# Kernel tuning notes

Measured on AMD Instinct MI355X. Metric: run time of the kernel, lower is better.

## Reference

```python
import jax, jax.numpy as jnp
import numpy as np

DIM = 1024
NUM_HEADS = 16
DH = DIM // NUM_HEADS  # 64
B, S = 4, 2048


def setup_inputs() -> dict:
    key = jax.random.key(0)
    ks = jax.random.split(key, 9)
    sc = 0.02
    x = jax.random.normal(ks[0], (B, S, DIM), dtype=jnp.float32)
    # per-head projection weights stacked: [H, DIM, DH] (input-major layout)
    Wq = jax.random.normal(ks[1], (NUM_HEADS, DIM, DH), dtype=jnp.float32) * sc
    Wk = jax.random.normal(ks[2], (NUM_HEADS, DIM, DH), dtype=jnp.float32) * sc
    Wv = jax.random.normal(ks[3], (NUM_HEADS, DIM, DH), dtype=jnp.float32) * sc
    bq = jax.random.normal(ks[4], (NUM_HEADS, DH), dtype=jnp.float32) * sc
    bk = jax.random.normal(ks[5], (NUM_HEADS, DH), dtype=jnp.float32) * sc
    bv = jax.random.normal(ks[6], (NUM_HEADS, DH), dtype=jnp.float32) * sc
    Wo = jax.random.normal(ks[7], (DIM, DIM), dtype=jnp.float32) * sc  # (in, out)
    bo = jax.random.normal(ks[8], (DIM,), dtype=jnp.float32) * sc
    return {"x": x, "Wq": Wq, "Wk": Wk, "Wv": Wv,
            "bq": bq, "bk": bk, "bv": bv, "Wo": Wo, "bo": bo}


def reference(x, Wq, Wk, Wv, bq, bk, bv, Wo, bo):
    # Per-head Linear projections, vectorized over heads: [B,H,S,DH]
    q = jnp.einsum('bsd,hde->bhse', x, Wq) + bq[None, :, None, :]
    k = jnp.einsum('bsd,hde->bhse', x, Wk) + bk[None, :, None, :]
    v = jnp.einsum('bsd,hde->bhse', x, Wv) + bv[None, :, None, :]
    # attention_matmul: Q @ K^T normalized by sqrt(dim_per_head)
    scale = 1.0 / jnp.sqrt(jnp.asarray(DH, dtype=x.dtype))
    scores = jnp.einsum('bhse,bhte->bhst', q, k) * scale  # [B,H,S,S]
    attn = jax.nn.softmax(scores, axis=-1)
    # attn_drop with p=0.0 is identity
    o = jnp.einsum('bhst,bhte->bhse', attn, v)  # [B,H,S,DH]
    # concat along last dim in head order -> [B,S,H*DH]
    o = jnp.transpose(o, (0, 2, 1, 3)).reshape(x.shape[0], x.shape[1], NUM_HEADS * DH)
    # output projection (proj_drop p=0.0 is identity)
    return o @ Wo + bo
```

## Files before the change

kernel.cpp:

```cpp
#include <hip/hip_runtime.h>
#include <stdint.h>

#define DIM 1024
#define NH 16
#define DH 64
#define BATCH 4
#define SEQ 2048
#define MROWS (BATCH*SEQ)

typedef _Float16 half8 __attribute__((ext_vector_type(8)));
typedef __fp16 fp16x2 __attribute__((ext_vector_type(2)));
typedef float f32x4 __attribute__((ext_vector_type(4)));
typedef float f32x16 __attribute__((ext_vector_type(16)));
typedef unsigned int u32x2 __attribute__((ext_vector_type(2)));

__device__ __forceinline__ unsigned short f2h(float f) {
    union { _Float16 h; unsigned short u; } c; c.h = (_Float16)f; return c.u;
}
__device__ __forceinline__ unsigned int pk2u(float a, float b) {
    union { fp16x2 h; unsigned int u; } c;
    c.h = __builtin_amdgcn_cvt_pkrtz(a, b);
    return c.u;
}
__device__ __forceinline__ float fexp2(float x) {
    return __builtin_amdgcn_exp2f(x);
}
__device__ __forceinline__ void gl_lds16(const unsigned short* g, unsigned short* l) {
    __builtin_amdgcn_global_load_lds(
        (__attribute__((address_space(1))) void*)(void*)g,
        (__attribute__((address_space(3))) void*)(void*)l,
        16, 0, 0);
}


__global__ void cast_x_kernel(const float* __restrict__ x,
                              unsigned short* __restrict__ xh, int n4) {
    int i = blockIdx.x * blockDim.x + threadIdx.x;
    if (i >= n4) return;
    float4 v = reinterpret_cast<const float4*>(x)[i];
    uint2 o;
    o.x = pk2u(v.x, v.y);
    o.y = pk2u(v.z, v.w);
    reinterpret_cast<uint2*>(xh)[i] = o;
}

__global__ __launch_bounds__(256) void prep_wqkv_kernel(
    const float* __restrict__ Wq, const float* __restrict__ Wk,
    const float* __restrict__ Wv, unsigned short* __restrict__ wt)
{
    __shared__ unsigned short tile[64][65];
    const int d0 = blockIdx.x * 64;
    const int h = blockIdx.y;
    const int mat = blockIdx.z;
    const float* W = (mat == 0) ? Wq : ((mat == 1) ? Wk : Wv);
    const int c = threadIdx.x & 63;
    const int rr = threadIdx.x >> 6;
#pragma unroll
    for (int p = 0; p < 16; p++) {
        int dl = p * 4 + rr;
        tile[dl][c] = f2h(W[((size_t)h * 1024 + d0 + dl) * 64 + c]);
    }
    __syncthreads();
#pragma unroll
    for (int p = 0; p < 16; p++) {
        int el = p * 4 + rr;
        wt[(((size_t)(mat * NH + h) * 64) + el) * DIM + d0 + c] = tile[c][el];
    }
}

__global__ __launch_bounds__(256) void prep_wo_kernel(
    const float* __restrict__ Wo, unsigned short* __restrict__ wot)
{
    __shared__ unsigned short tile[64][65];
    const int d0 = blockIdx.x * 64;
    const int o0 = blockIdx.y * 64;
    const int c = threadIdx.x & 63;
    const int rr = threadIdx.x >> 6;
#pragma unroll
    for (int p = 0; p < 16; p++) {
        int dl = p * 4 + rr;
        tile[dl][c] = f2h(Wo[(size_t)(d0 + dl) * DIM + o0 + c]);
    }
    __syncthreads();
#pragma unroll
    for (int p = 0; p < 16; p++) {
        int ol = p * 4 + rr;
        wot[(size_t)(o0 + ol) * DIM + d0 + c] = tile[c][ol];
    }
}

__global__ __launch_bounds__(256) void transpose_v_kernel(
    const unsigned short* __restrict__ Vb, unsigned short* __restrict__ Vt)
{
    __shared__ unsigned short tile[64][65];
    const int s0 = blockIdx.x * 64;
    const size_t bh = (size_t)blockIdx.z * NH + blockIdx.y;
    const int c = threadIdx.x & 63;
    const int rr = threadIdx.x >> 6;
    const unsigned short* src = Vb + bh * SEQ * DH;
    unsigned short* dst = Vt + bh * DH * SEQ;
#pragma unroll
    for (int p = 0; p < 16; p++) {
        int sl = p * 4 + rr;
        tile[sl][c] = src[(size_t)(s0 + sl) * DH + c];
    }
    __syncthreads();
#pragma unroll
    for (int p = 0; p < 16; p++) {
        int dr = p * 4 + rr;
        dst[(size_t)dr * SEQ + s0 + c] = tile[c][dr];
    }
}

__global__ __launch_bounds__(256) void qkv_gemm_kernel(
    const unsigned short* __restrict__ xh,
    const unsigned short* __restrict__ wt,
    const float* __restrict__ bq, const float* __restrict__ bk,
    const float* __restrict__ bv,
    unsigned short* __restrict__ Qb,
    unsigned short* __restrict__ Kb,
    unsigned short* __restrict__ Vb)
{
    const int rowblk = blockIdx.x;
    const int hpair = blockIdx.y;
    const int mat = blockIdx.z;
    const int wave = threadIdx.x >> 6;
    const int lane = threadIdx.x & 63;
    const int quad = lane >> 4;
    const int lr = lane & 15;
    const int mhalf = wave & 1;
    const int nhalf = wave >> 1;

    __shared__ __align__(16) unsigned short Ab[2][128 * 32];
    __shared__ __align__(16) unsigned short Bt[2][128 * 32];

    const unsigned short* Asrc = xh + (size_t)rowblk * 128 * DIM;
    const unsigned short* Bsrc = wt + (size_t)(mat * NH + hpair * 2) * DH * DIM;

    const int srow = lane >> 2;
    const int scs = lane & 3;

    f32x4 acc[4][4];
#pragma unroll
    for (int mt = 0; mt < 4; mt++)
#pragma unroll
        for (int nt = 0; nt < 4; nt++) acc[mt][nt] = (f32x4){0.f, 0.f, 0.f, 0.f};

    auto stage = [&](int k0, int sel) {
#pragma unroll
        for (int jj = 0; jj < 2; jj++) {
            const int j = wave * 2 + jj;
            const int r = j * 16 + srow;
            const int cg = scs ^ ((r >> 1) & 3);
            gl_lds16(Asrc + (size_t)r * DIM + k0 + cg * 8, &Ab[sel][j * 512]);
            gl_lds16(Bsrc + (size_t)r * DIM + k0 + cg * 8, &Bt[sel][j * 512]);
        }
    };

    stage(0, 0);
    __syncthreads();

    for (int i = 0; i < DIM / 32; i++) {
        const int sel = i & 1;
        if (i + 1 < DIM / 32) stage((i + 1) * 32, sel ^ 1);

        half8 af[4], bf[4];
#pragma unroll
        for (int mt = 0; mt < 4; mt++) {
            const int row = mhalf * 64 + mt * 16 + lr;
            const int slot = quad ^ ((row >> 1) & 3);
            af[mt] = *reinterpret_cast<const half8*>(&Ab[sel][row * 32 + slot * 8]);
        }
#pragma unroll
        for (int nt = 0; nt < 4; nt++) {
            const int row = nhalf * 64 + nt * 16 + lr;
            const int slot = quad ^ ((row >> 1) & 3);
            bf[nt] = *reinterpret_cast<const half8*>(&Bt[sel][row * 32 + slot * 8]);
        }
#pragma unroll
        for (int mt = 0; mt < 4; mt++)
#pragma unroll
            for (int nt = 0; nt < 4; nt++)
                acc[mt][nt] = __builtin_amdgcn_mfma_f32_16x16x32_f16(
                    af[mt], bf[nt], acc[mt][nt], 0, 0, 0);
        __syncthreads();
    }

    const float* bias = (mat == 0) ? bq : ((mat == 1) ? bk : bv);
    const float scale = (mat == 0) ? 0.1803368801111601f : 1.0f;
    unsigned short* outp = (mat == 0) ? Qb : ((mat == 1) ? Kb : Vb);
    const int rowBase = rowblk * 128 + mhalf * 64;
    const int bb = rowBase / SEQ;
    const int sBase = rowBase % SEQ;

#pragma unroll
    for (int mt = 0; mt < 4; mt++) {
        const int s0 = sBase + mt * 16 + quad * 4;
#pragma unroll
        for (int nt = 0; nt < 4; nt++) {
            const int e = nhalf * 64 + nt * 16 + lr;
            const int head = hpair * 2 + (e >> 6);
            const int n = e & 63;
            const float bvl = bias[head * DH + n];
            const size_t base = (size_t)(bb * NH + head) * SEQ * DH;
#pragma unroll
            for (int r = 0; r < 4; r++) {
                outp[base + (size_t)(s0 + r) * DH + n] = f2h((acc[mt][nt][r] + bvl) * scale);
            }
        }
    }
}

__global__ __launch_bounds__(256, 4) void attn_kernel(
    const unsigned short* __restrict__ Qb,
    const unsigned short* __restrict__ Kb,
    const unsigned short* __restrict__ Vt,
    unsigned short* __restrict__ Ob)
{
    const int h = blockIdx.y;
    const int bb = blockIdx.z;
    const int wave = threadIdx.x >> 6;
    const int lane = threadIdx.x & 63;
    const int ql = lane & 31;
    const int hi = lane >> 5;
    const int qBase = blockIdx.x * 128 + wave * 32;

    const size_t bh = (size_t)(bb * NH + h);
    const unsigned short* Qh = Qb + bh * SEQ * DH;
    const unsigned short* Kh = Kb + bh * SEQ * DH;
    const unsigned short* Vh = Vt + bh * DH * SEQ;

    __shared__ __align__(16) unsigned short Kbuf[2][64 * 64];
    __shared__ __align__(16) unsigned short Vbuf[2][64 * 64];

    const int srow = lane >> 3;
    const int scs = lane & 7;
    const int cg = scs ^ srow;
    int koff[2], voff[2];
#pragma unroll
    for (int jj = 0; jj < 2; jj++) {
        const int r = wave * 16 + jj * 8 + srow;
        koff[jj] = r * DH + cg * 8;
        voff[jj] = r * SEQ + cg * 8;
    }

    auto stage = [&](int kt, int sel) {
        gl_lds16(Kh + (size_t)kt * DH + koff[0], &Kbuf[sel][wave * 1024]);
        gl_lds16(Kh + (size_t)kt * DH + koff[1], &Kbuf[sel][wave * 1024 + 512]);
        gl_lds16(Vh + kt + voff[0], &Vbuf[sel][wave * 1024]);
        gl_lds16(Vh + kt + voff[1], &Vbuf[sel][wave * 1024 + 512]);
    };

    half8 qf[4];
#pragma unroll
    for (int ks = 0; ks < 4; ks++)
        qf[ks] = *reinterpret_cast<const half8*>(
            Qh + (size_t)(qBase + ql) * DH + ks * 16 + hi * 8);

    f32x16 z16;
#pragma unroll
    for (int e = 0; e < 16; e++) z16[e] = 0.f;

    f32x16 o[2];
#pragma unroll
    for (int mt = 0; mt < 2; mt++) o[mt] = z16;
    float lsA = 0.f, lsB = 0.f;

    auto compute = [&](int sel) {
        f32x16 sacc[2];
        __builtin_amdgcn_s_setprio(1);
#pragma unroll
        for (int ks = 0; ks < 4; ks++) {
#pragma unroll
            for (int kb = 0; kb < 2; kb++) {
                const int row = kb * 32 + ql;
                const int slot = (ks * 2 + hi) ^ (row & 7);
                half8 kf = *reinterpret_cast<const half8*>(&Kbuf[sel][row * 64 + slot * 8]);
                sacc[kb] = __builtin_amdgcn_mfma_f32_32x32x16_f16(
                    kf, qf[ks], ks ? sacc[kb] : z16, 0, 0, 0);
            }
        }
        __builtin_amdgcn_s_setprio(0);

        unsigned int pfu[4][4];
#pragma unroll
        for (int kb = 0; kb < 2; kb++) {
            unsigned int c[8];
#pragma unroll
            for (int m = 0; m < 8; m++) {
                float a = fexp2(sacc[kb][2 * m]);
                float b2 = fexp2(sacc[kb][2 * m + 1]);
                if (m & 1) lsB += a + b2; else lsA += a + b2;
                c[m] = pk2u(a, b2);
            }
#pragma unroll
            for (int ks = 0; ks < 2; ks++) {
                u32x2 w02 = __builtin_amdgcn_permlane32_swap(
                    c[4 * ks + 0], c[4 * ks + 2], false, false);
                u32x2 w13 = __builtin_amdgcn_permlane32_swap(
                    c[4 * ks + 1], c[4 * ks + 3], false, false);
                pfu[kb * 2 + ks][0] = w02[0];
                pfu[kb * 2 + ks][1] = w13[0];
                pfu[kb * 2 + ks][2] = w02[1];
                pfu[kb * 2 + ks][3] = w13[1];
            }
        }

        __builtin_amdgcn_s_setprio(1);
#pragma unroll
        for (int ks = 0; ks < 4; ks++) {
            union { unsigned int u[4]; half8 h; } cv;
            cv.u[0] = pfu[ks][0]; cv.u[1] = pfu[ks][1];
            cv.u[2] = pfu[ks][2]; cv.u[3] = pfu[ks][3];
            const half8 pf = cv.h;
#pragma unroll
            for (int mt = 0; mt < 2; mt++) {
                const int row = mt * 32 + ql;
                const int slot = (ks * 2 + hi) ^ (row & 7);
                half8 vf = *reinterpret_cast<const half8*>(&Vbuf[sel][row * 64 + slot * 8]);
                o[mt] = __builtin_amdgcn_mfma_f32_32x32x16_f16(
                    vf, pf, o[mt], 0, 0, 0);
            }
        }
        __builtin_amdgcn_s_setprio(0);
    };

    stage(0, 0);
    __syncthreads();

    for (int i = 0; i < SEQ / 64; i += 2) {
        stage((i + 1) * 64, 1);
        compute(0);
        __syncthreads();
        if (i + 2 < SEQ / 64) stage((i + 2) * 64, 0);
        compute(1);
        __syncthreads();
    }

    float l = lsA + lsB;
    l += __shfl_xor(l, 32);
    const float inv = 1.f / l;
    const size_t orow = (size_t)(bb * SEQ + qBase + ql) * DIM + h * DH;
#pragma unroll
    for (int mt = 0; mt < 2; mt++) {
#pragma unroll
        for (int g = 0; g < 4; g++) {
            uint2 pkd;
            pkd.x = pk2u(o[mt][4 * g + 0] * inv, o[mt][4 * g + 1] * inv);
            pkd.y = pk2u(o[mt][4 * g + 2] * inv, o[mt][4 * g + 3] * inv);
            *reinterpret_cast<uint2*>(Ob + orow + mt * 32 + 8 * g + 4 * hi) = pkd;
        }
    }
}

__global__ __launch_bounds__(256) void out_proj_kernel(
    const unsigned short* __restrict__ Ob,
    const unsigned short* __restrict__ wot,
    const float* __restrict__ bo,
    float* __restrict__ out)
{
    const int rowblk = blockIdx.x;
    const int colblk = blockIdx.y;
    const int wave = threadIdx.x >> 6;
    const int lane = threadIdx.x & 63;
    const int quad = lane >> 4;
    const int lr = lane & 15;
    const int mhalf = wave & 1;
    const int nhalf = wave >> 1;

    __shared__ __align__(16) unsigned short Ab[2][128 * 32];
    __shared__ __align__(16) unsigned short Bt[2][128 * 32];

    const unsigned short* Asrc = Ob + (size_t)rowblk * 128 * DIM;
    const unsigned short* Bsrc = wot + (size_t)colblk * 128 * DIM;

    const int srow = lane >> 2;
    const int scs = lane & 3;

    f32x4 acc[4][4];
#pragma unroll
    for (int mt = 0; mt < 4; mt++)
#pragma unroll
        for (int nt = 0; nt < 4; nt++) acc[mt][nt] = (f32x4){0.f, 0.f, 0.f, 0.f};

    auto stage = [&](int k0, int sel) {
#pragma unroll
        for (int jj = 0; jj < 2; jj++) {
            const int j = wave * 2 + jj;
            const int r = j * 16 + srow;
            const int cg = scs ^ ((r >> 1) & 3);
            gl_lds16(Asrc + (size_t)r * DIM + k0 + cg * 8, &Ab[sel][j * 512]);
            gl_lds16(Bsrc + (size_t)r * DIM + k0 + cg * 8, &Bt[sel][j * 512]);
        }
    };

    stage(0, 0);
    __syncthreads();

    for (int i = 0; i < DIM / 32; i++) {
        const int sel = i & 1;
        if (i + 1 < DIM / 32) stage((i + 1) * 32, sel ^ 1);

        half8 af[4], bf[4];
#pragma unroll
        for (int mt = 0; mt < 4; mt++) {
            const int row = mhalf * 64 + mt * 16 + lr;
            const int slot = quad ^ ((row >> 1) & 3);
            af[mt] = *reinterpret_cast<const half8*>(&Ab[sel][row * 32 + slot * 8]);
        }
#pragma unroll
        for (int nt = 0; nt < 4; nt++) {
            const int row = nhalf * 64 + nt * 16 + lr;
            const int slot = quad ^ ((row >> 1) & 3);
            bf[nt] = *reinterpret_cast<const half8*>(&Bt[sel][row * 32 + slot * 8]);
        }
#pragma unroll
        for (int mt = 0; mt < 4; mt++)
#pragma unroll
            for (int nt = 0; nt < 4; nt++)
                acc[mt][nt] = __builtin_amdgcn_mfma_f32_16x16x32_f16(
                    af[mt], bf[nt], acc[mt][nt], 0, 0, 0);
        __syncthreads();
    }

    const int rowBase = rowblk * 128 + mhalf * 64;
    const int colBase = colblk * 128 + nhalf * 64;
#pragma unroll
    for (int mt = 0; mt < 4; mt++) {
#pragma unroll
        for (int nt = 0; nt < 4; nt++) {
            const int col = colBase + nt * 16 + lr;
            const float bias = bo[col];
#pragma unroll
            for (int r = 0; r < 4; r++) {
                int row = rowBase + mt * 16 + quad * 4 + r;
                out[(size_t)row * DIM + col] = acc[mt][nt][r] + bias;
            }
        }
    }
}


extern "C" void kernel_launch(void* const* d_in, const int* in_sizes, int n_in,
                              void* d_out, int out_size, void* d_ws, size_t ws_size,
                              hipStream_t stream) {
    const float* x  = (const float*)d_in[0];
    const float* Wq = (const float*)d_in[1];
    const float* Wk = (const float*)d_in[2];
    const float* Wv = (const float*)d_in[3];
    const float* bq = (const float*)d_in[4];
    const float* bk = (const float*)d_in[5];
    const float* bv = (const float*)d_in[6];
    const float* Wo = (const float*)d_in[7];
    const float* bo = (const float*)d_in[8];
    float* out = (float*)d_out;

    unsigned short* xh  = (unsigned short*)d_ws;
    unsigned short* wt  = xh  + (size_t)MROWS * DIM;
    unsigned short* wot = wt  + (size_t)3 * NH * DH * DIM;
    unsigned short* Qb  = wot + (size_t)DIM * DIM;
    unsigned short* Kb  = Qb  + (size_t)BATCH * NH * SEQ * DH;
    unsigned short* Vb  = Kb  + (size_t)BATCH * NH * SEQ * DH;
    unsigned short* Vt  = Vb  + (size_t)BATCH * NH * SEQ * DH;
    unsigned short* Ob  = Vt  + (size_t)BATCH * NH * SEQ * DH;

    {
        int n4 = MROWS * DIM / 4;
        cast_x_kernel<<<(n4 + 255) / 256, 256, 0, stream>>>(x, xh, n4);
    }
    prep_wqkv_kernel<<<dim3(16, NH, 3), 256, 0, stream>>>(Wq, Wk, Wv, wt);
    prep_wo_kernel<<<dim3(16, 16), 256, 0, stream>>>(Wo, wot);
    qkv_gemm_kernel<<<dim3(64, 8, 3), 256, 0, stream>>>(xh, wt, bq, bk, bv, Qb, Kb, Vb);
    transpose_v_kernel<<<dim3(SEQ / 64, NH, BATCH), 256, 0, stream>>>(Vb, Vt);
    attn_kernel<<<dim3(SEQ / 128, NH, BATCH), 256, 0, stream>>>(Qb, Kb, Vt, Ob);
    out_proj_kernel<<<dim3(64, 8), 256, 0, stream>>>(Ob, wot, bo, out);
}
```

Baseline: 310.0 us.

## Software-pipeline attention: overlap next tile's QK^T with previous tile's PV MFMAs

Restructures the attention inner loop so each iteration computes S=QK^T for tile i while issuing the PV MFMAs for tile i-1 from the previous probabilities held in registers. K and V staging are split and offset by one tile, with a prologue and an epilogue to drain the last PV. The LDS swizzle also gains an extra XOR term based on row bits, meant to cut bank conflicts, and slot offsets are precomputed. This is meant to hide the exp/permlane softmax latency behind MFMA work, at the cost of more live registers (pf[4]).

```diff
diff --git a/kernel.cpp b/kernel.cpp
--- a/kernel.cpp
+++ b/kernel.cpp
@@ -235,20 +235,24 @@
 
     const int srow = lane >> 3;
     const int scs = lane & 7;
-    const int cg = scs ^ srow;
     int koff[2], voff[2];
 #pragma unroll
     for (int jj = 0; jj < 2; jj++) {
         const int r = wave * 16 + jj * 8 + srow;
+        const int cg = scs ^ srow ^ ((wave * 2 + jj) & 3);
         koff[jj] = r * DH + cg * 8;
         voff[jj] = r * SEQ + cg * 8;
     }
 
-    auto stage = [&](int kt, int sel) {
-        gl_lds16(Kh + (size_t)kt * DH + koff[0], &Kbuf[sel][wave * 1024]);
-        gl_lds16(Kh + (size_t)kt * DH + koff[1], &Kbuf[sel][wave * 1024 + 512]);
-        gl_lds16(Vh + kt + voff[0], &Vbuf[sel][wave * 1024]);
-        gl_lds16(Vh + kt + voff[1], &Vbuf[sel][wave * 1024 + 512]);
+    auto stage_k = [&](int kt, int sel) {
+        const size_t base = (size_t)kt * 64 * DH;
+        gl_lds16(Kh + base + koff[0], &Kbuf[sel][wave * 1024]);
+        gl_lds16(Kh + base + koff[1], &Kbuf[sel][wave * 1024 + 512]);
+    };
+    auto stage_v = [&](int kt, int sel) {
+        const size_t base = (size_t)kt * 64;
+        gl_lds16(Vh + base + voff[0], &Vbuf[sel][wave * 1024]);
+        gl_lds16(Vh + base + voff[1], &Vbuf[sel][wave * 1024 + 512]);
     };
 
     half8 qf[4];
@@ -257,6 +261,13 @@
         qf[ks] = *reinterpret_cast<const half8*>(
             Qh + (size_t)(qBase + ql) * DH + ks * 16 + hi * 8);
 
+    const int slotx = (ql & 7) ^ ((ql >> 3) & 3);
+    int rowb[2], soff[4];
+#pragma unroll
+    for (int b = 0; b < 2; b++) rowb[b] = (b * 32 + ql) * 64;
+#pragma unroll
+    for (int ks = 0; ks < 4; ks++) soff[ks] = ((ks * 2 + hi) ^ slotx) * 8;
+
     f32x16 z16;
 #pragma unroll
     for (int e = 0; e < 16; e++) z16[e] = 0.f;
@@ -265,24 +276,32 @@
 #pragma unroll
     for (int mt = 0; mt < 2; mt++) o[mt] = z16;
     float lsA = 0.f, lsB = 0.f;
-
-    auto compute = [&](int sel) {
+    half8 pf[4];
+
+    auto burst = [&](int sel, bool doPV) {
         f32x16 sacc[2];
         __builtin_amdgcn_s_setprio(1);
 #pragma unroll
         for (int ks = 0; ks < 4; ks++) {
 #pragma unroll
-            for (int kb = 0; kb < 2; kb++) {
-                const int row = kb * 32 + ql;
-                const int slot = (ks * 2 + hi) ^ (row & 7);
-                half8 kf = *reinterpret_cast<const half8*>(&Kbuf[sel][row * 64 + slot * 8]);
-                sacc[kb] = __builtin_amdgcn_mfma_f32_32x32x16_f16(
-                    kf, qf[ks], ks ? sacc[kb] : z16, 0, 0, 0);
+            for (int b = 0; b < 2; b++) {
+                half8 kf = *reinterpret_cast<const half8*>(
+                    &Kbuf[sel][rowb[b] + soff[ks]]);
+                sacc[b] = __builtin_amdgcn_mfma_f32_32x32x16_f16(
+                    kf, qf[ks], ks ? sacc[b] : z16, 0, 0, 0);
+            }
+            if (doPV) {
+#pragma unroll
+                for (int mt = 0; mt < 2; mt++) {
+                    half8 vf = *reinterpret_cast<const half8*>(
+                        &Vbuf[sel][rowb[mt] + soff[ks]]);
+                    o[mt] = __builtin_amdgcn_mfma_f32_32x32x16_f16(
+                        vf, pf[ks], o[mt], 0, 0, 0);
+                }
             }
         }
         __builtin_amdgcn_s_setprio(0);
 
-        unsigned int pfu[4][4];
 #pragma unroll
         for (int kb = 0; kb < 2; kb++) {
             unsigned int c[8];
@@ -299,43 +318,41 @@
                     c[4 * ks + 0], c[4 * ks + 2], false, false);
                 u32x2 w13 = __builtin_amdgcn_permlane32_swap(
                     c[4 * ks + 1], c[4 * ks + 3], false, false);
-                pfu[kb * 2 + ks][0] = w02[0];
-                pfu[kb * 2 + ks][1] = w13[0];
-                pfu[kb * 2 + ks][2] = w02[1];
-                pfu[kb * 2 + ks][3] = w13[1];
-            }
-        }
-
-        __builtin_amdgcn_s_setprio(1);
-#pragma unroll
-        for (int ks = 0; ks < 4; ks++) {
-            union { unsigned int u[4]; half8 h; } cv;
-            cv.u[0] = pfu[ks][0]; cv.u[1] = pfu[ks][1];
-            cv.u[2] = pfu[ks][2]; cv.u[3] = pfu[ks][3];
-            const half8 pf = cv.h;
-#pragma unroll
-            for (int mt = 0; mt < 2; mt++) {
-                const int row = mt * 32 + ql;
-                const int slot = (ks * 2 + hi) ^ (row & 7);
-                half8 vf = *reinterpret_cast<const half8*>(&Vbuf[sel][row * 64 + slot * 8]);
-                o[mt] = __builtin_amdgcn_mfma_f32_32x32x16_f16(
-                    vf, pf, o[mt], 0, 0, 0);
-            }
-        }
-        __builtin_amdgcn_s_setprio(0);
+                union { unsigned int u[4]; half8 h; } cv;
+                cv.u[0] = w02[0]; cv.u[1] = w13[0];
+                cv.u[2] = w02[1]; cv.u[3] = w13[1];
+                pf[kb * 2 + ks] = cv.h;
+            }
+        }
     };
 
-    stage(0, 0);
-    __syncthreads();
-
-    for (int i = 0; i < SEQ / 64; i += 2) {
-        stage((i + 1) * 64, 1);
-        compute(0);
+    stage_k(0, 0);
+    __syncthreads();
+
+    stage_k(1, 1);
+    stage_v(0, 1);
+    burst(0, false);
+    __syncthreads();
+
+    for (int i = 1; i < SEQ / 64; i++) {
+        const int sel = i & 1;
+        if (i + 1 < SEQ / 64) stage_k(i + 1, sel ^ 1);
+        stage_v(i, sel ^ 1);
+        burst(sel, true);
         __syncthreads();
-        if (i + 2 < SEQ / 64) stage((i + 2) * 64, 0);
-        compute(1);
-        __syncthreads();
-    }
+    }
+
+    __builtin_amdgcn_s_setprio(1);
+#pragma unroll
+    for (int ks = 0; ks < 4; ks++)
+#pragma unroll
+        for (int mt = 0; mt < 2; mt++) {
+            half8 vf = *reinterpret_cast<const half8*>(
+                &Vbuf[0][rowb[mt] + soff[ks]]);
+            o[mt] = __builtin_amdgcn_mfma_f32_32x32x16_f16(
+                vf, pf[ks], o[mt], 0, 0, 0);
+        }
+    __builtin_amdgcn_s_setprio(0);
 
     float l = lsA + lsB;
     l += __shfl_xor(l, 32);
```

Result: no change. 310.3 us (+0.1%).
